# Kernel optimization log

Hardware: AMD Instinct MI355X
Metric: run time of the kernel (lower is better)

## Reference

```python
import jax, jax.numpy as jnp
import numpy as np

D_MODEL = 256
N_LAYERS = 4
D_STATE = 16
D_CONV = 4
D_INNER = 2 * D_MODEL          # expand=2
DT_RANK = (D_MODEL + 15) // 16  # 'auto' -> ceil(d_model/16) = 16
NUM_CLASSES = 10
BATCH = 4
HW = 32


def setup_inputs() -> dict:
    key = jax.random.key(0)
    ks = jax.random.split(key, 16)
    std = 0.02
    inp = {}
    inp["x"] = jax.random.normal(ks[0], (BATCH, 3, HW, HW), dtype=jnp.float32)
    inp["input_proj_w"] = std * jax.random.normal(ks[1], (D_MODEL, 3), dtype=jnp.float32)
    inp["input_proj_b"] = jnp.zeros((D_MODEL,), jnp.float32)
    inp["in_proj_w"] = std * jax.random.normal(ks[2], (N_LAYERS, 2 * D_INNER, D_MODEL), dtype=jnp.float32)
    inp["conv_w"] = std * jax.random.normal(ks[3], (N_LAYERS, D_INNER, D_CONV), dtype=jnp.float32)
    inp["conv_b"] = jnp.zeros((N_LAYERS, D_INNER), jnp.float32)
    inp["x_proj_w"] = std * jax.random.normal(ks[4], (N_LAYERS, DT_RANK + 2 * D_STATE, D_INNER), dtype=jnp.float32)
    inp["dt_proj_w"] = std * jax.random.normal(ks[5], (N_LAYERS, D_INNER, DT_RANK), dtype=jnp.float32)
    # dt bias ~ inverse-softplus of small dt values (Mamba-style init)
    inp["dt_proj_b"] = jnp.log(jnp.expm1(0.01 * jnp.ones((N_LAYERS, D_INNER), jnp.float32)))
    # A_log init: log(1..d_state) per channel (Mamba S4D-real init)
    a = jnp.log(jnp.arange(1, D_STATE + 1, dtype=jnp.float32))
    inp["A_log"] = jnp.broadcast_to(a, (N_LAYERS, D_INNER, D_STATE)).copy()
    inp["D_skip"] = jnp.ones((N_LAYERS, D_INNER), jnp.float32)
    inp["out_proj_w"] = std * jax.random.normal(ks[6], (N_LAYERS, D_MODEL, D_INNER), dtype=jnp.float32)
    inp["ln_w"] = jnp.ones((N_LAYERS, D_MODEL), jnp.float32)
    inp["ln_b"] = jnp.zeros((N_LAYERS, D_MODEL), jnp.float32)
    inp["fn_w"] = jnp.ones((D_MODEL,), jnp.float32)
    inp["fn_b"] = jnp.zeros((D_MODEL,), jnp.float32)
    inp["cls_w"] = std * jax.random.normal(ks[7], (NUM_CLASSES, D_MODEL), dtype=jnp.float32)
    inp["cls_b"] = jnp.zeros((NUM_CLASSES,), jnp.float32)
    return inp


def _layer_norm(x, w, b, eps=1e-5):
    mu = jnp.mean(x, axis=-1, keepdims=True)
    var = jnp.mean(jnp.square(x - mu), axis=-1, keepdims=True)
    return (x - mu) * jax.lax.rsqrt(var + eps) * w + b


def _mamba_block(x, in_w, cw, cb, xp_w, dt_w, dt_b, A_log, D_skip, out_w):
    B_, L, _ = x.shape
    xz = jnp.einsum('bld,ed->ble', x, in_w)            # [B,L,2*Din]
    xh, z = jnp.split(xz, 2, axis=-1)                  # [B,L,Din] each
    # depthwise causal conv1d (kernel D_CONV, left pad D_CONV-1)
    xp = jnp.pad(xh, ((0, 0), (D_CONV - 1, 0), (0, 0)))
    conv = cb + sum(xp[:, k:k + L, :] * cw[:, k] for k in range(D_CONV))
    xh = jax.nn.silu(conv)
    x_dbl = jnp.einsum('bld,ed->ble', xh, xp_w)        # [B,L,dt_rank+2N]
    dt, Bm, Cm = jnp.split(x_dbl, [DT_RANK, DT_RANK + D_STATE], axis=-1)
    delta = jax.nn.softplus(jnp.einsum('blr,dr->bld', dt, dt_w) + dt_b)  # [B,L,Din]
    A = -jnp.exp(A_log)                                # [Din,N]
    deltaA = jnp.exp(delta[..., None] * A)             # [B,L,Din,N]
    deltaBu = delta[..., None] * Bm[:, :, None, :] * xh[..., None]       # [B,L,Din,N]

    def step(h, inputs):
        dA_t, dBu_t, C_t = inputs
        h = dA_t * h + dBu_t                           # [B,Din,N]
        y = jnp.einsum('bdn,bn->bd', h, C_t)
        return h, y

    h0 = jnp.zeros((B_, D_INNER, D_STATE), x.dtype)
    _, ys = jax.lax.scan(step, h0, (deltaA.transpose(1, 0, 2, 3),
                                    deltaBu.transpose(1, 0, 2, 3),
                                    Cm.transpose(1, 0, 2)))
    y = ys.transpose(1, 0, 2) + xh * D_skip            # [B,L,Din]
    y = y * jax.nn.silu(z)
    return jnp.einsum('bld,od->blo', y, out_w)         # [B,L,Dmodel]


def reference(x, input_proj_w, input_proj_b, in_proj_w, conv_w, conv_b,
              x_proj_w, dt_proj_w, dt_proj_b, A_log, D_skip, out_proj_w,
              ln_w, ln_b, fn_w, fn_b, cls_w, cls_b):
    B_ = x.shape[0]
    seq = x.transpose(0, 2, 3, 1).reshape(B_, -1, 3)   # [B, H*W, 3]
    h = jnp.einsum('blc,dc->bld', seq, input_proj_w) + input_proj_b
    for i in range(N_LAYERS):
        res = h
        h = _layer_norm(h, ln_w[i], ln_b[i])
        h = _mamba_block(h, in_proj_w[i], conv_w[i], conv_b[i], x_proj_w[i],
                         dt_proj_w[i], dt_proj_b[i], A_log[i], D_skip[i], out_proj_w[i])
        h = h + res  # dropout is identity (p=0 / eval)
    h = jnp.mean(h, axis=1)                            # [B, Dmodel]
    h = _layer_norm(h, fn_w, fn_b)
    return h @ cls_w.T + cls_b                         # [B, num_classes]
```

## Files before the change

### kernel.cpp

```cpp
#include <hip/hip_runtime.h>
#include <math.h>

#define B_ 4
#define L_ 1024
#define DM 256
#define DIN 512
#define NST 16
#define DTR 16
#define CHK 64
#define CT (L_ / CHK)

typedef short short8 __attribute__((ext_vector_type(8)));
typedef float float4v __attribute__((ext_vector_type(4)));

__device__ __forceinline__ float softplusf(float x) {
    return (x > 20.f) ? x : log1pf(__expf(x));
}
__device__ __forceinline__ float siluf(float x) {
    return x / (1.f + __expf(-x));
}
__device__ __forceinline__ unsigned short f2bf(float f) {
    unsigned int u = __float_as_uint(f);
    u = (u + 0x7fffu + ((u >> 16) & 1u)) >> 16;
    return (unsigned short)u;
}

__device__ __forceinline__ void block_reduce2(float& a, float& q) {
    #pragma unroll
    for (int off = 32; off > 0; off >>= 1) {
        a += __shfl_down(a, off);
        q += __shfl_down(q, off);
    }
    __shared__ float sa[4], sq[4];
    int lane = threadIdx.x & 63, w = threadIdx.x >> 6;
    if (lane == 0) { sa[w] = a; sq[w] = q; }
    __syncthreads();
    a = sa[0] + sa[1] + sa[2] + sa[3];
    q = sq[0] + sq[1] + sq[2] + sq[3];
}

__global__ __launch_bounds__(256) void prologue_kernel(
    const float* __restrict__ inw, int na, const float* __restrict__ xpw, int nb,
    const float* __restrict__ opw, int nc,
    unsigned short* __restrict__ oa, unsigned short* __restrict__ ob,
    unsigned short* __restrict__ oc, int nconv,
    const float* __restrict__ x, const float* __restrict__ ipw,
    const float* __restrict__ ipb, float* __restrict__ h0)
{
    if ((int)blockIdx.x < nconv) {
        int i = blockIdx.x * 256 + threadIdx.x;
        if (i < na) { oa[i] = f2bf(inw[i]); return; }
        int j = i - na;
        if (j < nb) { ob[j] = f2bf(xpw[j]); return; }
        int k = j - nb;
        if (k < nc) oc[k] = f2bf(opw[k]);
        return;
    }
    int idx = (blockIdx.x - nconv) * 256 + threadIdx.x;
    int d = idx & (DM - 1);
    int bl = idx >> 8;
    int l = bl & (L_ - 1);
    int b = bl >> 10;
    const float* xb = x + (size_t)b * 3 * L_;
    float acc = ipb[d];
    acc = fmaf(xb[0 * L_ + l], ipw[d * 3 + 0], acc);
    acc = fmaf(xb[1 * L_ + l], ipw[d * 3 + 1], acc);
    acc = fmaf(xb[2 * L_ + l], ipw[d * 3 + 2], acc);
    h0[idx] = acc;
}

__global__ __launch_bounds__(256) void gemm_in_ln(
    const float* __restrict__ A, const unsigned short* __restrict__ W,
    const float* __restrict__ lw, const float* __restrict__ lb,
    float* __restrict__ C, int N)
{
    __shared__ unsigned short As[64][264];
    __shared__ unsigned short Ws[64][72];
    const int tid = threadIdx.x;
    const int wave = tid >> 6;
    const int lane = tid & 63;
    const int m_l = lane & 15;
    const int q = lane >> 4;
    const int m0 = blockIdx.y * 64;
    const int n0 = blockIdx.x * 64;

    {
        const int rg = lane >> 4;
        const int c4 = lane & 15;
        #pragma unroll
        for (int p = 0; p < 4; ++p) {
            int r = p * 16 + wave * 4 + rg;
            const float* ap = A + (size_t)(m0 + r) * DM;
            float4 v[4];
            float s = 0.f, qq = 0.f;
            #pragma unroll
            for (int i = 0; i < 4; ++i) {
                v[i] = *(const float4*)(ap + i * 64 + c4 * 4);
                s  += v[i].x + v[i].y + v[i].z + v[i].w;
                qq += v[i].x * v[i].x + v[i].y * v[i].y
                    + v[i].z * v[i].z + v[i].w * v[i].w;
            }
            s += __shfl_xor(s, 1); qq += __shfl_xor(qq, 1);
            s += __shfl_xor(s, 2); qq += __shfl_xor(qq, 2);
            s += __shfl_xor(s, 4); qq += __shfl_xor(qq, 4);
            s += __shfl_xor(s, 8); qq += __shfl_xor(qq, 8);
            float mu = s * (1.f / DM);
            float var = qq * (1.f / DM) - mu * mu;
            float rs = rsqrtf(var + 1e-5f);
            #pragma unroll
            for (int i = 0; i < 4; ++i) {
                int col = i * 64 + c4 * 4;
                float4 wv = *(const float4*)(lw + col);
                float4 bv = *(const float4*)(lb + col);
                unsigned short* dst = &As[r][col];
                dst[0] = f2bf((v[i].x - mu) * rs * wv.x + bv.x);
                dst[1] = f2bf((v[i].y - mu) * rs * wv.y + bv.y);
                dst[2] = f2bf((v[i].z - mu) * rs * wv.z + bv.z);
                dst[3] = f2bf((v[i].w - mu) * rs * wv.w + bv.w);
            }
        }
    }
    __syncthreads();

    const int sr = tid >> 3;
    const int sc = (tid & 7) * 8;
    float4v acc[4];
    #pragma unroll
    for (int j = 0; j < 4; ++j) acc[j] = (float4v)(0.f);

    for (int k0 = 0; k0 < DM; k0 += 64) {
        *(short8*)&Ws[sr][sc]      = *(const short8*)(W + (size_t)(n0 + sr) * DM + k0 + sc);
        *(short8*)&Ws[sr + 32][sc] = *(const short8*)(W + (size_t)(n0 + sr + 32) * DM + k0 + sc);
        __syncthreads();
        #pragma unroll
        for (int kk = 0; kk < 64; kk += 32) {
            short8 a = *(const short8*)&As[wave * 16 + m_l][k0 + kk + q * 8];
            #pragma unroll
            for (int j4 = 0; j4 < 4; ++j4) {
                short8 b = *(const short8*)&Ws[j4 * 16 + m_l][kk + q * 8];
                acc[j4] = __builtin_amdgcn_mfma_f32_16x16x32_bf16(a, b, acc[j4], 0, 0, 0);
            }
        }
        __syncthreads();
    }
    #pragma unroll
    for (int j4 = 0; j4 < 4; ++j4) {
        int n = n0 + j4 * 16 + m_l;
        #pragma unroll
        for (int reg = 0; reg < 4; ++reg) {
            int m = m0 + wave * 16 + q * 4 + reg;
            C[(size_t)m * N + n] = acc[j4][reg];
        }
    }
}

__global__ __launch_bounds__(512) void conv_xproj_summary(
    const float* __restrict__ xz, const float* __restrict__ cw,
    const float* __restrict__ cb, const unsigned short* __restrict__ W,
    const float* __restrict__ A_log, const float* __restrict__ dt_w,
    const float* __restrict__ dt_b,
    float* __restrict__ dbc, float* __restrict__ S, float* __restrict__ H)
{
    __shared__ unsigned short As[CT][520];
    __shared__ float Dbc[CT][64];
    const int tid = threadIdx.x;
    const int d = tid;
    const int c = blockIdx.x;
    const int b = blockIdx.y;
    const int l0 = c * CT;

    float xcr[CT];
    {
        const float w0 = cw[d * 4 + 0], w1 = cw[d * 4 + 1];
        const float w2 = cw[d * 4 + 2], w3 = cw[d * 4 + 3];
        const float cbv = cb[d];
        const float* xp = xz + ((size_t)(b * L_ + l0)) * (2 * DIN) + d;
        float x0 = 0.f, x1 = 0.f, x2 = 0.f;
        if (l0 >= 3) {
            x0 = xp[(ptrdiff_t)(-3) * (2 * DIN)];
            x1 = xp[(ptrdiff_t)(-2) * (2 * DIN)];
            x2 = xp[(ptrdiff_t)(-1) * (2 * DIN)];
        }
        #pragma unroll
        for (int t = 0; t < CT; ++t) {
            float x3 = xp[(size_t)t * (2 * DIN)];
            float a = fmaf(x0, w0, cbv);
            a = fmaf(x1, w1, a);
            a = fmaf(x2, w2, a);
            a = fmaf(x3, w3, a);
            float v = siluf(a);
            xcr[t] = v;
            As[t][d] = f2bf(v);
            x0 = x1; x1 = x2; x2 = x3;
        }
    }
    __syncthreads();

    {
        const int wave = tid >> 6;
        const int lane = tid & 63;
        const int m_l = lane & 15;
        const int q = lane >> 4;
        if (wave < 3) {
            float4v acc = (float4v)(0.f);
            for (int k0 = 0; k0 < DIN; k0 += 32) {
                short8 a  = *(const short8*)&As[m_l][k0 + q * 8];
                short8 bf = *(const short8*)(W + (size_t)(wave * 16 + m_l) * DIN + k0 + q * 8);
                acc = __builtin_amdgcn_mfma_f32_16x16x32_bf16(a, bf, acc, 0, 0, 0);
            }
            #pragma unroll
            for (int reg = 0; reg < 4; ++reg)
                Dbc[q * 4 + reg][wave * 16 + m_l] = acc[reg];
        }
    }
    __syncthreads();

    for (int i = tid; i < CT * 48; i += 512) {
        int t = i / 48, col = i - t * 48;
        dbc[((size_t)(b * L_ + l0 + t)) * 48 + col] = Dbc[t][col];
    }

    float A[NST], tw[DTR];
    #pragma unroll
    for (int j = 0; j < NST; ++j) A[j] = -__expf(A_log[d * NST + j]);
    #pragma unroll
    for (int r = 0; r < DTR; ++r) tw[r] = dt_w[d * DTR + r];
    const float tb = dt_b[d];
    float h[NST];
    #pragma unroll
    for (int j = 0; j < NST; ++j) h[j] = 0.f;
    float ssum = 0.f;
    #pragma unroll 4
    for (int t = 0; t < CT; ++t) {
        float acc = tb;
        #pragma unroll
        for (int r = 0; r < DTR; ++r) acc = fmaf(Dbc[t][r], tw[r], acc);
        float dlt = softplusf(acc);
        float t0 = dlt * xcr[t];
        ssum += dlt;
        #pragma unroll
        for (int j = 0; j < NST; ++j) {
            float dA = __expf(A[j] * dlt);
            h[j] = fmaf(dA, h[j], t0 * Dbc[t][DTR + j]);
        }
    }
    S[((size_t)b * CHK + c) * DIN + d] = ssum;
    float* Hp = H + (((size_t)b * CHK + c) * NST) * DIN + d;
    #pragma unroll
    for (int j = 0; j < NST; ++j)
        Hp[(size_t)j * DIN] = h[j];
}

__global__ __launch_bounds__(256) void scan_prefix_kernel(
    const float* __restrict__ S, float* __restrict__ H,
    const float* __restrict__ A_log)
{
    int idx = blockIdx.x * 256 + threadIdx.x;
    int d = idx & (DIN - 1);
    int n = (idx >> 9) & (NST - 1);
    int b = idx >> 13;
    float A = -__expf(A_log[d * NST + n]);
    float hprev = 0.f;
    const float* Sp = S + (size_t)b * CHK * DIN + d;
    float* Hp = H + (((size_t)b * CHK) * NST + n) * DIN + d;
    for (int c = 0; c < CHK; ++c) {
        float Hc = Hp[(size_t)c * NST * DIN];
        float Sc = Sp[(size_t)c * DIN];
        Hp[(size_t)c * NST * DIN] = hprev;
        hprev = fmaf(__expf(A * Sc), hprev, Hc);
    }
}

__global__ __launch_bounds__(256) void scan_apply_kernel(
    const float* __restrict__ dbc, const float* __restrict__ xz,
    const float* __restrict__ cw, const float* __restrict__ cb,
    const float* __restrict__ A_log, const float* __restrict__ dt_w,
    const float* __restrict__ dt_b, const float* __restrict__ Dskip,
    const float* __restrict__ H, unsigned short* __restrict__ y)
{
    const int d = blockIdx.x * 256 + threadIdx.x;
    const int c = blockIdx.y;
    const int b = blockIdx.z;
    float A[NST], tw[DTR];
    #pragma unroll
    for (int j = 0; j < NST; ++j) A[j] = -__expf(A_log[d * NST + j]);
    #pragma unroll
    for (int r = 0; r < DTR; ++r) tw[r] = dt_w[d * DTR + r];
    const float tb = dt_b[d];
    const float Dsk = Dskip[d];
    const int l0 = c * CT;
    const float* bc = dbc + ((size_t)(b * L_ + l0)) * 48;
    const float* xp = xz  + ((size_t)(b * L_ + l0)) * (2 * DIN) + d;
    const float* zp = xp + DIN;
    unsigned short* yp = y + ((size_t)(b * L_ + l0)) * DIN + d;

    const float w0 = cw[d * 4 + 0], w1 = cw[d * 4 + 1];
    const float w2 = cw[d * 4 + 2], w3 = cw[d * 4 + 3];
    const float cbv = cb[d];
    float x0 = 0.f, x1 = 0.f, x2 = 0.f;
    if (l0 >= 3) {
        x0 = xp[(ptrdiff_t)(-3) * (2 * DIN)];
        x1 = xp[(ptrdiff_t)(-2) * (2 * DIN)];
        x2 = xp[(ptrdiff_t)(-1) * (2 * DIN)];
    }

    float h[NST];
    const float* Hp = H + (((size_t)b * CHK + c) * NST) * DIN + d;
    #pragma unroll
    for (int j = 0; j < NST; ++j) h[j] = Hp[(size_t)j * DIN];

    #pragma unroll 4
    for (int t = 0; t < CT; ++t) {
        float x3 = xp[(size_t)t * (2 * DIN)];
        float ca = fmaf(x0, w0, cbv);
        ca = fmaf(x1, w1, ca);
        ca = fmaf(x2, w2, ca);
        ca = fmaf(x3, w3, ca);
        float xcv = siluf(ca);
        x0 = x1; x1 = x2; x2 = x3;

        const float* br = bc + t * 48;
        float acc = tb;
        #pragma unroll
        for (int r = 0; r < DTR; ++r) acc = fmaf(br[r], tw[r], acc);
        float dlt = softplusf(acc);
        float zv  = zp[(size_t)t * (2 * DIN)];
        float t0 = dlt * xcv;
        float p = 0.f;
        #pragma unroll
        for (int j = 0; j < NST; ++j) {
            float dA = __expf(A[j] * dlt);
            h[j] = fmaf(dA, h[j], t0 * br[DTR + j]);
            p = fmaf(h[j], br[DTR + NST + j], p);
        }
        yp[t * DIN] = f2bf((p + xcv * Dsk) * siluf(zv));
    }
}

__global__ __launch_bounds__(256) void gemm_bt_bf16(
    const unsigned short* __restrict__ A, const unsigned short* __restrict__ W,
    float* C, int M, int N, int K, int lda, int accumulate)
{
    __shared__ unsigned short As[64][72];
    __shared__ unsigned short Ws[64][72];
    const int tid = threadIdx.x;
    const int wave = tid >> 6;
    const int lane = tid & 63;
    const int m_l = lane & 15;
    const int q = lane >> 4;
    const int m0 = blockIdx.y * 64;
    const int n0 = blockIdx.x * 64;
    const int sr = tid >> 3;
    const int sc = (tid & 7) * 8;

    float4v acc[4];
    #pragma unroll
    for (int j = 0; j < 4; ++j) acc[j] = (float4v)(0.f);

    for (int k0 = 0; k0 < K; k0 += 64) {
        *(short8*)&As[sr][sc]      = *(const short8*)(A + (size_t)(m0 + sr) * lda + k0 + sc);
        *(short8*)&As[sr + 32][sc] = *(const short8*)(A + (size_t)(m0 + sr + 32) * lda + k0 + sc);
        short8 wz = (short8)0;
        int wn0 = n0 + sr, wn1 = n0 + sr + 32;
        *(short8*)&Ws[sr][sc]      = (wn0 < N) ? *(const short8*)(W + (size_t)wn0 * K + k0 + sc) : wz;
        *(short8*)&Ws[sr + 32][sc] = (wn1 < N) ? *(const short8*)(W + (size_t)wn1 * K + k0 + sc) : wz;
        __syncthreads();
        #pragma unroll
        for (int kk = 0; kk < 64; kk += 32) {
            short8 a = *(const short8*)&As[wave * 16 + m_l][kk + q * 8];
            #pragma unroll
            for (int j4 = 0; j4 < 4; ++j4) {
                short8 bf = *(const short8*)&Ws[j4 * 16 + m_l][kk + q * 8];
                acc[j4] = __builtin_amdgcn_mfma_f32_16x16x32_bf16(a, bf, acc[j4], 0, 0, 0);
            }
        }
        __syncthreads();
    }
    #pragma unroll
    for (int j4 = 0; j4 < 4; ++j4) {
        int n = n0 + j4 * 16 + m_l;
        if (n < N) {
            #pragma unroll
            for (int reg = 0; reg < 4; ++reg) {
                int m = m0 + wave * 16 + q * 4 + reg;
                float* cp = C + (size_t)m * N + n;
                if (accumulate) *cp += acc[j4][reg];
                else            *cp  = acc[j4][reg];
            }
        }
    }
}

__global__ __launch_bounds__(256) void head_partial_kernel(
    const float* __restrict__ h, float* __restrict__ partial)
{
    int b = blockIdx.x >> 4, ch = blockIdx.x & 15, t = threadIdx.x;
    const float* hp = h + ((size_t)(b * L_ + ch * 64)) * DM + t;
    float s = 0.f;
    #pragma unroll 8
    for (int l = 0; l < 64; ++l) s += hp[(size_t)l * DM];
    partial[(size_t)blockIdx.x * DM + t] = s;
}

__global__ __launch_bounds__(256) void head_final_kernel(
    const float* __restrict__ partial, const float* __restrict__ fn_w,
    const float* __restrict__ fn_b, const float* __restrict__ cls_w,
    const float* __restrict__ cls_b, float* __restrict__ out)
{
    int b = blockIdx.x, t = threadIdx.x;
    const float* pp = partial + (size_t)b * 16 * DM + t;
    float s = 0.f;
    #pragma unroll
    for (int c = 0; c < 16; ++c) s += pp[(size_t)c * DM];
    s *= (1.f / L_);
    float a = s, q = s * s;
    block_reduce2(a, q);
    float mu = a * (1.f / DM);
    float var = q * (1.f / DM) - mu * mu;
    float v = (s - mu) * rsqrtf(var + 1e-5f) * fn_w[t] + fn_b[t];
    __shared__ float pooled[DM];
    pooled[t] = v;
    __syncthreads();
    if (t < 10) {
        float acc = cls_b[t];
        for (int d2 = 0; d2 < DM; ++d2)
            acc = fmaf(pooled[d2], cls_w[t * DM + d2], acc);
        out[b * 10 + t] = acc;
    }
}

extern "C" void kernel_launch(void* const* d_in, const int* in_sizes, int n_in,
                              void* d_out, int out_size, void* d_ws, size_t ws_size,
                              hipStream_t stream)
{
    const float* x    = (const float*)d_in[0];
    const float* ipw  = (const float*)d_in[1];
    const float* ipb  = (const float*)d_in[2];
    const float* inw  = (const float*)d_in[3];
    const float* cw   = (const float*)d_in[4];
    const float* cb   = (const float*)d_in[5];
    const float* xpw  = (const float*)d_in[6];
    const float* dtw  = (const float*)d_in[7];
    const float* dtb  = (const float*)d_in[8];
    const float* alog = (const float*)d_in[9];
    const float* dsk  = (const float*)d_in[10];
    const float* opw  = (const float*)d_in[11];
    const float* lnw  = (const float*)d_in[12];
    const float* lnb  = (const float*)d_in[13];
    const float* fnw  = (const float*)d_in[14];
    const float* fnb  = (const float*)d_in[15];
    const float* clw  = (const float*)d_in[16];
    const float* clb  = (const float*)d_in[17];

    float* ws     = (float*)d_ws;
    float* hbuf   = ws;
    float* xzbuf  = hbuf   + (size_t)B_ * L_ * DM;
    float* dbcbuf = xzbuf  + (size_t)B_ * L_ * 2 * DIN;
    float* Sbuf   = dbcbuf + (size_t)B_ * L_ * 48;
    float* Hbuf   = Sbuf   + (size_t)B_ * CHK * DIN;
    float* tail   = Hbuf   + (size_t)B_ * CHK * NST * DIN;
    unsigned short* yb16  = (unsigned short*)tail;
    unsigned short* inw16 = yb16  + (size_t)B_ * L_ * DIN;
    unsigned short* xpw16 = inw16 + (size_t)4 * 1024 * DM;
    unsigned short* opw16 = xpw16 + (size_t)4 * 48 * DIN;
    float* partial = (float*)(opw16 + (size_t)4 * DM * DIN);

    const int BL = B_ * L_;
    const int NIN = 4 * 1024 * DM, NXP = 4 * 48 * DIN, NOP = 4 * DM * DIN;
    const int NCONV = (NIN + NXP + NOP + 255) / 256;

    prologue_kernel<<<NCONV + BL * DM / 256, 256, 0, stream>>>(
        inw, NIN, xpw, NXP, opw, NOP, inw16, xpw16, opw16, NCONV,
        x, ipw, ipb, hbuf);

    for (int i = 0; i < 4; ++i) {
        gemm_in_ln<<<dim3(2 * DIN / 64, BL / 64), 256, 0, stream>>>(
            hbuf, inw16 + (size_t)i * 1024 * DM, lnw + i * DM, lnb + i * DM,
            xzbuf, 2 * DIN);
        conv_xproj_summary<<<dim3(CHK, B_), 512, 0, stream>>>(
            xzbuf, cw + i * DIN * 4, cb + i * DIN,
            xpw16 + (size_t)i * 48 * DIN, alog + i * DIN * NST,
            dtw + i * DIN * DTR, dtb + i * DIN, dbcbuf, Sbuf, Hbuf);
        scan_prefix_kernel<<<B_ * NST * DIN / 256, 256, 0, stream>>>(
            Sbuf, Hbuf, alog + i * DIN * NST);
        scan_apply_kernel<<<dim3(DIN / 256, CHK, B_), 256, 0, stream>>>(
            dbcbuf, xzbuf, cw + i * DIN * 4, cb + i * DIN,
            alog + i * DIN * NST, dtw + i * DIN * DTR, dtb + i * DIN,
            dsk + i * DIN, Hbuf, yb16);
        gemm_bt_bf16<<<dim3(DM / 64, BL / 64), 256, 0, stream>>>(
            yb16, opw16 + (size_t)i * DM * DIN, hbuf, BL, DM, DIN, DIN, 1);
    }

    head_partial_kernel<<<B_ * 16, 256, 0, stream>>>(hbuf, partial);
    head_final_kernel<<<B_, 256, 0, stream>>>(partial, fnw, fnb, clw, clb,
                                              (float*)d_out);
}
```

Before: 421.0 us.

## Fuse out-projection GEMM into scan apply kernel via shared-memory y tile

```diff
diff --git a/kernel.cpp b/kernel.cpp
--- a/kernel.cpp
+++ b/kernel.cpp
@@ -271,121 +271,95 @@
     }
 }
 
-__global__ __launch_bounds__(256) void scan_apply_kernel(
+__global__ __launch_bounds__(512) void scan_apply_out(
     const float* __restrict__ dbc, const float* __restrict__ xz,
     const float* __restrict__ cw, const float* __restrict__ cb,
     const float* __restrict__ A_log, const float* __restrict__ dt_w,
     const float* __restrict__ dt_b, const float* __restrict__ Dskip,
-    const float* __restrict__ H, unsigned short* __restrict__ y)
-{
-    const int d = blockIdx.x * 256 + threadIdx.x;
-    const int c = blockIdx.y;
-    const int b = blockIdx.z;
-    float A[NST], tw[DTR];
-    #pragma unroll
-    for (int j = 0; j < NST; ++j) A[j] = -__expf(A_log[d * NST + j]);
-    #pragma unroll
-    for (int r = 0; r < DTR; ++r) tw[r] = dt_w[d * DTR + r];
-    const float tb = dt_b[d];
-    const float Dsk = Dskip[d];
+    const float* __restrict__ H, const unsigned short* __restrict__ Wout,
+    float* __restrict__ hbuf)
+{
+    __shared__ unsigned short Ys[CT][520];
+    const int tid = threadIdx.x;
+    const int d = tid;
+    const int c = blockIdx.x;
+    const int b = blockIdx.y;
     const int l0 = c * CT;
-    const float* bc = dbc + ((size_t)(b * L_ + l0)) * 48;
-    const float* xp = xz  + ((size_t)(b * L_ + l0)) * (2 * DIN) + d;
-    const float* zp = xp + DIN;
-    unsigned short* yp = y + ((size_t)(b * L_ + l0)) * DIN + d;
-
-    const float w0 = cw[d * 4 + 0], w1 = cw[d * 4 + 1];
-    const float w2 = cw[d * 4 + 2], w3 = cw[d * 4 + 3];
-    const float cbv = cb[d];
-    float x0 = 0.f, x1 = 0.f, x2 = 0.f;
-    if (l0 >= 3) {
-        x0 = xp[(ptrdiff_t)(-3) * (2 * DIN)];
-        x1 = xp[(ptrdiff_t)(-2) * (2 * DIN)];
-        x2 = xp[(ptrdiff_t)(-1) * (2 * DIN)];
-    }
-
-    float h[NST];
-    const float* Hp = H + (((size_t)b * CHK + c) * NST) * DIN + d;
-    #pragma unroll
-    for (int j = 0; j < NST; ++j) h[j] = Hp[(size_t)j * DIN];
-
-    #pragma unroll 4
-    for (int t = 0; t < CT; ++t) {
-        float x3 = xp[(size_t)t * (2 * DIN)];
-        float ca = fmaf(x0, w0, cbv);
-        ca = fmaf(x1, w1, ca);
-        ca = fmaf(x2, w2, ca);
-        ca = fmaf(x3, w3, ca);
-        float xcv = siluf(ca);
-        x0 = x1; x1 = x2; x2 = x3;
-
-        const float* br = bc + t * 48;
-        float acc = tb;
-        #pragma unroll
-        for (int r = 0; r < DTR; ++r) acc = fmaf(br[r], tw[r], acc);
-        float dlt = softplusf(acc);
-        float zv  = zp[(size_t)t * (2 * DIN)];
-        float t0 = dlt * xcv;
-        float p = 0.f;
-        #pragma unroll
-        for (int j = 0; j < NST; ++j) {
-            float dA = __expf(A[j] * dlt);
-            h[j] = fmaf(dA, h[j], t0 * br[DTR + j]);
-            p = fmaf(h[j], br[DTR + NST + j], p);
-        }
-        yp[t * DIN] = f2bf((p + xcv * Dsk) * siluf(zv));
-    }
-}
-
-__global__ __launch_bounds__(256) void gemm_bt_bf16(
-    const unsigned short* __restrict__ A, const unsigned short* __restrict__ W,
-    float* C, int M, int N, int K, int lda, int accumulate)
-{
-    __shared__ unsigned short As[64][72];
-    __shared__ unsigned short Ws[64][72];
-    const int tid = threadIdx.x;
-    const int wave = tid >> 6;
-    const int lane = tid & 63;
-    const int m_l = lane & 15;
-    const int q = lane >> 4;
-    const int m0 = blockIdx.y * 64;
-    const int n0 = blockIdx.x * 64;
-    const int sr = tid >> 3;
-    const int sc = (tid & 7) * 8;
-
-    float4v acc[4];
-    #pragma unroll
-    for (int j = 0; j < 4; ++j) acc[j] = (float4v)(0.f);
-
-    for (int k0 = 0; k0 < K; k0 += 64) {
-        *(short8*)&As[sr][sc]      = *(const short8*)(A + (size_t)(m0 + sr) * lda + k0 + sc);
-        *(short8*)&As[sr + 32][sc] = *(const short8*)(A + (size_t)(m0 + sr + 32) * lda + k0 + sc);
-        short8 wz = (short8)0;
-        int wn0 = n0 + sr, wn1 = n0 + sr + 32;
-        *(short8*)&Ws[sr][sc]      = (wn0 < N) ? *(const short8*)(W + (size_t)wn0 * K + k0 + sc) : wz;
-        *(short8*)&Ws[sr + 32][sc] = (wn1 < N) ? *(const short8*)(W + (size_t)wn1 * K + k0 + sc) : wz;
-        __syncthreads();
-        #pragma unroll
-        for (int kk = 0; kk < 64; kk += 32) {
-            short8 a = *(const short8*)&As[wave * 16 + m_l][kk + q * 8];
-            #pragma unroll
-            for (int j4 = 0; j4 < 4; ++j4) {
-                short8 bf = *(const short8*)&Ws[j4 * 16 + m_l][kk + q * 8];
-                acc[j4] = __builtin_amdgcn_mfma_f32_16x16x32_bf16(a, bf, acc[j4], 0, 0, 0);
-            }
-        }
-        __syncthreads();
-    }
-    #pragma unroll
-    for (int j4 = 0; j4 < 4; ++j4) {
-        int n = n0 + j4 * 16 + m_l;
-        if (n < N) {
+
+    {
+        float A[NST], tw[DTR];
+        #pragma unroll
+        for (int j = 0; j < NST; ++j) A[j] = -__expf(A_log[d * NST + j]);
+        #pragma unroll
+        for (int r = 0; r < DTR; ++r) tw[r] = dt_w[d * DTR + r];
+        const float tb = dt_b[d];
+        const float Dsk = Dskip[d];
+        const float* bc = dbc + ((size_t)(b * L_ + l0)) * 48;
+        const float* xp = xz  + ((size_t)(b * L_ + l0)) * (2 * DIN) + d;
+        const float* zp = xp + DIN;
+
+        const float w0 = cw[d * 4 + 0], w1 = cw[d * 4 + 1];
+        const float w2 = cw[d * 4 + 2], w3 = cw[d * 4 + 3];
+        const float cbv = cb[d];
+        float x0 = 0.f, x1 = 0.f, x2 = 0.f;
+        if (l0 >= 3) {
+            x0 = xp[(ptrdiff_t)(-3) * (2 * DIN)];
+            x1 = xp[(ptrdiff_t)(-2) * (2 * DIN)];
+            x2 = xp[(ptrdiff_t)(-1) * (2 * DIN)];
+        }
+
+        float h[NST];
+        const float* Hp = H + (((size_t)b * CHK + c) * NST) * DIN + d;
+        #pragma unroll
+        for (int j = 0; j < NST; ++j) h[j] = Hp[(size_t)j * DIN];
+
+        #pragma unroll 4
+        for (int t = 0; t < CT; ++t) {
+            float x3 = xp[(size_t)t * (2 * DIN)];
+            float ca = fmaf(x0, w0, cbv);
+            ca = fmaf(x1, w1, ca);
+            ca = fmaf(x2, w2, ca);
+            ca = fmaf(x3, w3, ca);
+            float xcv = siluf(ca);
+            x0 = x1; x1 = x2; x2 = x3;
+
+            const float* br = bc + t * 48;
+            float acc = tb;
+            #pragma unroll
+            for (int r = 0; r < DTR; ++r) acc = fmaf(br[r], tw[r], acc);
+            float dlt = softplusf(acc);
+            float zv  = zp[(size_t)t * (2 * DIN)];
+            float t0 = dlt * xcv;
+            float p = 0.f;
+            #pragma unroll
+            for (int j = 0; j < NST; ++j) {
+                float dA = __expf(A[j] * dlt);
+                h[j] = fmaf(dA, h[j], t0 * br[DTR + j]);
+                p = fmaf(h[j], br[DTR + NST + j], p);
+            }
+            Ys[t][d] = f2bf((p + xcv * Dsk) * siluf(zv));
+        }
+    }
+    __syncthreads();
+
+    {
+        const int wave = tid >> 6;
+        const int lane = tid & 63;
+        const int m_l = lane & 15;
+        const int q = lane >> 4;
+        #pragma unroll
+        for (int nt = 0; nt < 2; ++nt) {
+            const int n0 = (wave * 2 + nt) * 16;
+            float4v acc = (float4v)(0.f);
+            for (int k0 = 0; k0 < DIN; k0 += 32) {
+                short8 a = *(const short8*)&Ys[m_l][k0 + q * 8];
+                short8 w = *(const short8*)(Wout + (size_t)(n0 + m_l) * DIN + k0 + q * 8);
+                acc = __builtin_amdgcn_mfma_f32_16x16x32_bf16(a, w, acc, 0, 0, 0);
+            }
             #pragma unroll
             for (int reg = 0; reg < 4; ++reg) {
-                int m = m0 + wave * 16 + q * 4 + reg;
-                float* cp = C + (size_t)m * N + n;
-                if (accumulate) *cp += acc[j4][reg];
-                else            *cp  = acc[j4][reg];
+                int row = q * 4 + reg;
+                hbuf[((size_t)(b * L_ + l0 + row)) * DM + n0 + m_l] += acc[reg];
             }
         }
     }
@@ -459,8 +433,7 @@
     float* Sbuf   = dbcbuf + (size_t)B_ * L_ * 48;
     float* Hbuf   = Sbuf   + (size_t)B_ * CHK * DIN;
     float* tail   = Hbuf   + (size_t)B_ * CHK * NST * DIN;
-    unsigned short* yb16  = (unsigned short*)tail;
-    unsigned short* inw16 = yb16  + (size_t)B_ * L_ * DIN;
+    unsigned short* inw16 = (unsigned short*)tail;
     unsigned short* xpw16 = inw16 + (size_t)4 * 1024 * DM;
     unsigned short* opw16 = xpw16 + (size_t)4 * 48 * DIN;
     float* partial = (float*)(opw16 + (size_t)4 * DM * DIN);
@@ -483,12 +456,10 @@
             dtw + i * DIN * DTR, dtb + i * DIN, dbcbuf, Sbuf, Hbuf);
         scan_prefix_kernel<<<B_ * NST * DIN / 256, 256, 0, stream>>>(
             Sbuf, Hbuf, alog + i * DIN * NST);
-        scan_apply_kernel<<<dim3(DIN / 256, CHK, B_), 256, 0, stream>>>(
+        scan_apply_out<<<dim3(CHK, B_), 512, 0, stream>>>(
             dbcbuf, xzbuf, cw + i * DIN * 4, cb + i * DIN,
             alog + i * DIN * NST, dtw + i * DIN * DTR, dtb + i * DIN,
-            dsk + i * DIN, Hbuf, yb16);
-        gemm_bt_bf16<<<dim3(DM / 64, BL / 64), 256, 0, stream>>>(
-            yb16, opw16 + (size_t)i * DM * DIN, hbuf, BL, DM, DIN, DIN, 1);
+            dsk + i * DIN, Hbuf, opw16 + (size_t)i * DM * DIN, hbuf);
     }
 
     head_partial_kernel<<<B_ * 16, 256, 0, stream>>>(hbuf, partial);
```

Result: faster. 385.6 us (-8.4%).
